# Kernel optimization log

Hardware: AMD Instinct MI355X
Metric: run time of the kernel (lower is better)

The kernel has to match this reference:

```python
import jax, jax.numpy as jnp
import numpy as np

B, N, NID, V, GH, PHI, RHO = 8, 256, 64, 128, 128, 256, 128
BN = B * N
EPS = 1e-5


def _layernorm(x, g, b):
    m = jnp.mean(x, axis=-1, keepdims=True)
    v = jnp.var(x, axis=-1, keepdims=True)
    return (x - m) * jax.lax.rsqrt(v + EPS) * g + b


def _edges(A):
    # dense adjacency -> flat batched edge list, exactly as mask.nonzero() ordering
    bidx = jnp.arange(B)[:, None, None]
    ii = jnp.arange(N)[None, :, None]
    jj = jnp.arange(N)[None, None, :]
    src = jnp.broadcast_to(bidx * N + ii, (B, N, N)).reshape(-1)  # edge_index[0] = b*N+i
    tgt = jnp.broadcast_to(bidx * N + jj, (B, N, N)).reshape(-1)  # edge_index[1] = b*N+j
    w = A.reshape(-1)
    valid = w != 0
    rel = (w > 0).astype(jnp.int32)
    return src, tgt, w, valid, rel


def _rgcn(H, src, tgt, valid, rel, Wrel, Wroot, bias):
    # torch_geometric RGCNConv: mean aggregation per relation at target + root + bias
    x_src = H[src]  # (E, d) gather
    out = H @ Wroot + bias
    for r in range(2):
        m = (valid & (rel == r)).astype(H.dtype)  # (E,)
        s = jax.ops.segment_sum(x_src * m[:, None], tgt, num_segments=BN)
        c = jax.ops.segment_sum(m, tgt, num_segments=BN)
        out = out + (s / jnp.maximum(c, 1.0)[:, None]) @ Wrel[r]
    return out


def setup_inputs() -> dict:
    key = jax.random.key(0)
    ks = jax.random.split(key, 24)
    p = lambda k, shape: jax.random.normal(k, shape, dtype=jnp.float32) * 0.02
    z = lambda *shape: jnp.zeros(shape, jnp.float32)
    return {
        "A": jax.random.normal(ks[0], (B, N, N), dtype=jnp.float32),
        "X": jax.random.normal(ks[1], (B, N, NID), dtype=jnp.float32),
        "home_mask": (jax.random.uniform(ks[2], (B, N)) > 0.5).astype(jnp.float32),
        "emb1_w": p(ks[3], (NID, V)), "emb1_b": z(V),
        "emb2_w": p(ks[4], (V, V)), "emb2_b": z(V),
        "rgcn_w_0": p(ks[5], (2, V, GH)), "rgcn_root_0": p(ks[6], (V, GH)), "rgcn_bias_0": z(GH),
        "lina_w_0": p(ks[7], (GH, GH)), "lina_b_0": z(GH),
        "linb_w_0": p(ks[8], (GH, GH)), "linb_b_0": z(GH),
        "rgcn_w_1": p(ks[9], (2, GH, GH)), "rgcn_root_1": p(ks[10], (GH, GH)), "rgcn_bias_1": z(GH),
        "lina_w_1": p(ks[11], (GH, GH)), "lina_b_1": z(GH),
        "linb_w_1": p(ks[12], (GH, GH)), "linb_b_1": z(GH),
        "norm_g": jnp.ones((GH,), jnp.float32), "norm_b": z(GH),
        "phi_w1": p(ks[13], (GH, PHI)), "phi_b1": z(PHI),
        "phi_w2": p(ks[14], (PHI, PHI)), "phi_b2": z(PHI),
        "rho_w1": p(ks[15], (PHI, RHO)), "rho_b1": z(RHO),
        "rho_w2": p(ks[16], (RHO, 1)), "rho_b2": z(1),
    }


def reference(A, X, home_mask, emb1_w, emb1_b, emb2_w, emb2_b,
              rgcn_w_0, rgcn_root_0, rgcn_bias_0, lina_w_0, lina_b_0, linb_w_0, linb_b_0,
              rgcn_w_1, rgcn_root_1, rgcn_bias_1, lina_w_1, lina_b_1, linb_w_1, linb_b_1,
              norm_g, norm_b, phi_w1, phi_b1, phi_w2, phi_b2,
              rho_w1, rho_b1, rho_w2, rho_b2):
    away_mask = 1.0 - home_mask
    H = jax.nn.relu(X @ emb1_w + emb1_b)
    H = (H @ emb2_w + emb2_b).reshape(BN, V)

    src, tgt, w, valid, rel = _edges(A)
    aw = jnp.abs(w) * valid.astype(w.dtype)  # |edge_weight|, zero for masked-out edges

    blocks = [
        (rgcn_w_0, rgcn_root_0, rgcn_bias_0, lina_w_0, lina_b_0, linb_w_0, linb_b_0),
        (rgcn_w_1, rgcn_root_1, rgcn_bias_1, lina_w_1, lina_b_1, linb_w_1, linb_b_1),
    ]
    agg = jnp.zeros_like(H)
    for (Wrel, Wroot, bias, law, lab, lbw, lbb) in blocks:
        H = H + agg
        H2 = _rgcn(H, src, tgt, valid, rel, Wrel, Wroot, bias)
        # gather-scale-scatter: agg[src] += H2[tgt] * |w|
        agg = jax.ops.segment_sum(H2[tgt] * aw[:, None], src, num_segments=BN)
        agg = jax.nn.relu(_layernorm(agg, norm_g, norm_b))  # dropout = identity (eval)
        agg = jax.nn.relu(agg @ law + lab)
        agg = agg @ lbw + lbb
    H = (H + agg).reshape(B, N, GH)

    # DeepSet phi (dropout = identity)
    h = jax.nn.relu(H @ phi_w1 + phi_b1)
    phi_out = jax.nn.relu(h @ phi_w2 + phi_b2)  # (B, N, PHI)

    home_sum = jnp.sum(phi_out * home_mask[:, :, None], axis=1)
    away_sum = jnp.sum(phi_out * away_mask[:, :, None], axis=1)

    def rho(s):
        return (jax.nn.relu(s @ rho_w1 + rho_b1) @ rho_w2 + rho_b2)[:, 0]

    out = rho(home_sum) - rho(away_sum)
    return 0.5 + 0.5 * jnp.tanh(out)  # (B,)
```

## Files before the change

### kernel.cpp

```cpp
#include <hip/hip_runtime.h>
#include <math.h>

#define NB 8

__global__ __launch_bounds__(256, 2) void k_embed(const float* __restrict__ X,
        const float* __restrict__ w1, const float* __restrict__ b1,
        const float* __restrict__ w2, const float* __restrict__ b2,
        float* __restrict__ H, float* __restrict__ pools) {
    const int r0 = blockIdx.x * 4;
    const int t = threadIdx.x, q = t & 31, u = t >> 5;
    __shared__ __align__(16) float part[4096];
    __shared__ __align__(16) float xq[256];
    __shared__ __align__(16) float h1q[512];
    if (blockIdx.x < 16) pools[blockIdx.x * 256 + t] = 0.f;
    if (t < 64) {
        float4 v;
        v.x = X[(size_t)(r0 + 0) * 64 + t];
        v.y = X[(size_t)(r0 + 1) * 64 + t];
        v.z = X[(size_t)(r0 + 2) * 64 + t];
        v.w = X[(size_t)(r0 + 3) * 64 + t];
        *(float4*)&xq[t * 4] = v;
    }
    __syncthreads();
    {
        float acc[16];
        #pragma unroll
        for (int i = 0; i < 16; ++i) acc[i] = 0.f;
        #pragma unroll
        for (int kk = 0; kk < 8; ++kk) {
            int k = u * 8 + kk;
            float4 w4 = *(const float4*)&w1[(size_t)k * 128 + q * 4];
            float wc[4] = {w4.x, w4.y, w4.z, w4.w};
            float4 x4 = *(const float4*)&xq[k * 4];
            float xr[4] = {x4.x, x4.y, x4.z, x4.w};
            #pragma unroll
            for (int r = 0; r < 4; ++r)
                #pragma unroll
                for (int c = 0; c < 4; ++c)
                    acc[r * 4 + c] = fmaf(xr[r], wc[c], acc[r * 4 + c]);
        }
        #pragma unroll
        for (int r = 0; r < 4; ++r)
            *(float4*)&part[u * 512 + r * 128 + q * 4] =
                make_float4(acc[r*4+0], acc[r*4+1], acc[r*4+2], acc[r*4+3]);
    }
    __syncthreads();
    if (t < 128) {
        int r = t >> 5, fq = t & 31;
        float4 s = *(const float4*)&b1[fq * 4];
        #pragma unroll
        for (int uu = 0; uu < 8; ++uu) {
            float4 p = *(const float4*)&part[uu * 512 + r * 128 + fq * 4];
            s.x += p.x; s.y += p.y; s.z += p.z; s.w += p.w;
        }
        h1q[(fq * 4 + 0) * 4 + r] = fmaxf(s.x, 0.f);
        h1q[(fq * 4 + 1) * 4 + r] = fmaxf(s.y, 0.f);
        h1q[(fq * 4 + 2) * 4 + r] = fmaxf(s.z, 0.f);
        h1q[(fq * 4 + 3) * 4 + r] = fmaxf(s.w, 0.f);
    }
    __syncthreads();
    {
        float a2[16];
        #pragma unroll
        for (int i = 0; i < 16; ++i) a2[i] = 0.f;
        #pragma unroll 8
        for (int kk = 0; kk < 16; ++kk) {
            int k = u * 16 + kk;
            float4 w4 = *(const float4*)&w2[(size_t)k * 128 + q * 4];
            float wc[4] = {w4.x, w4.y, w4.z, w4.w};
            float4 h4 = *(const float4*)&h1q[k * 4];
            float hr[4] = {h4.x, h4.y, h4.z, h4.w};
            #pragma unroll
            for (int r = 0; r < 4; ++r)
                #pragma unroll
                for (int c = 0; c < 4; ++c)
                    a2[r * 4 + c] = fmaf(hr[r], wc[c], a2[r * 4 + c]);
        }
        #pragma unroll
        for (int r = 0; r < 4; ++r)
            *(float4*)&part[u * 512 + r * 128 + q * 4] =
                make_float4(a2[r*4+0], a2[r*4+1], a2[r*4+2], a2[r*4+3]);
    }
    __syncthreads();
    if (t < 128) {
        int r = t >> 5, fq = t & 31;
        float4 s = *(const float4*)&b2[fq * 4];
        #pragma unroll
        for (int uu = 0; uu < 8; ++uu) {
            float4 p = *(const float4*)&part[uu * 512 + r * 128 + fq * 4];
            s.x += p.x; s.y += p.y; s.z += p.z; s.w += p.w;
        }
        *(float4*)&H[(size_t)(r0 + r) * 128 + fq * 4] = s;
    }
}

__global__ __launch_bounds__(256, 2) void k_gcn1(
        const float* __restrict__ A, const float* __restrict__ H,
        const float* __restrict__ Wrel, const float* __restrict__ Wroot,
        const float* __restrict__ bias, float* __restrict__ H2) {
    const int b  = blockIdx.x >> 6;
    const int j0 = (blockIdx.x & 63) * 4;
    const int t = threadIdx.x, q = t & 31, u = t >> 5;
    __shared__ __align__(16) float maskM[2048];
    __shared__ __align__(16) float part[8192];
    __shared__ __align__(16) float pb[1536];
    __shared__ float cntp[256];
    __shared__ float cnt[8];
    const float* Ab = A + (size_t)b * 65536;
    const float* Hb = H + (size_t)b * 32768;
    const float* W0 = Wrel;
    const float* W1 = Wrel + 16384;

    {
        float4 a = *(const float4*)(Ab + (size_t)t * 256 + j0);
        float4 m0, m1;
        m0.x = (a.x < 0.f) ? 1.f : 0.f; m1.x = (a.x > 0.f) ? 1.f : 0.f;
        m0.y = (a.y < 0.f) ? 1.f : 0.f; m1.y = (a.y > 0.f) ? 1.f : 0.f;
        m0.z = (a.z < 0.f) ? 1.f : 0.f; m1.z = (a.z > 0.f) ? 1.f : 0.f;
        m0.w = (a.w < 0.f) ? 1.f : 0.f; m1.w = (a.w > 0.f) ? 1.f : 0.f;
        *(float4*)&maskM[t * 8]     = m0;
        *(float4*)&maskM[t * 8 + 4] = m1;
    }
    __syncthreads();
    {
        int chunk = t >> 3, slot = t & 7;
        float c = 0.f;
        #pragma unroll
        for (int qq = 0; qq < 8; ++qq) c += maskM[(chunk * 8 + qq) * 8 + slot];
        cntp[slot * 32 + chunk] = c;
    }
    float acc0[16], acc1[16];
    #pragma unroll
    for (int i = 0; i < 16; ++i) { acc0[i] = 0.f; acc1[i] = 0.f; }
    #pragma unroll 8
    for (int ii = 0; ii < 32; ++ii) {
        int i = u * 32 + ii;
        float4 h4 = *(const float4*)&Hb[(size_t)i * 128 + q * 4];
        float hc[4] = {h4.x, h4.y, h4.z, h4.w};
        float4 m0 = *(const float4*)&maskM[i * 8];
        float4 m1 = *(const float4*)&maskM[i * 8 + 4];
        float mr0[4] = {m0.x, m0.y, m0.z, m0.w};
        float mr1[4] = {m1.x, m1.y, m1.z, m1.w};
        #pragma unroll
        for (int r = 0; r < 4; ++r)
            #pragma unroll
            for (int c = 0; c < 4; ++c) {
                acc0[r * 4 + c] = fmaf(mr0[r], hc[c], acc0[r * 4 + c]);
                acc1[r * 4 + c] = fmaf(mr1[r], hc[c], acc1[r * 4 + c]);
            }
    }
    #pragma unroll
    for (int r = 0; r < 4; ++r) {
        *(float4*)&part[u * 1024 + r * 128 + q * 4] =
            make_float4(acc0[r*4+0], acc0[r*4+1], acc0[r*4+2], acc0[r*4+3]);
        *(float4*)&part[u * 1024 + (4 + r) * 128 + q * 4] =
            make_float4(acc1[r*4+0], acc1[r*4+1], acc1[r*4+2], acc1[r*4+3]);
    }
    if (t < 8) {
        float s = 0.f;
        #pragma unroll
        for (int c = 0; c < 32; ++c) s += cntp[t * 32 + c];
        cnt[t] = s;
    }
    __syncthreads();
    {
        int slot = t >> 5, fq = t & 31;
        float4 s = make_float4(0.f, 0.f, 0.f, 0.f);
        #pragma unroll
        for (int uu = 0; uu < 8; ++uu) {
            float4 p = *(const float4*)&part[uu * 1024 + slot * 128 + fq * 4];
            s.x += p.x; s.y += p.y; s.z += p.z; s.w += p.w;
        }
        float rc = 1.f / fmaxf(cnt[slot], 1.f);
        pb[(fq * 4 + 0) * 12 + 4 + slot] = s.x * rc;
        pb[(fq * 4 + 1) * 12 + 4 + slot] = s.y * rc;
        pb[(fq * 4 + 2) * 12 + 4 + slot] = s.z * rc;
        pb[(fq * 4 + 3) * 12 + 4 + slot] = s.w * rc;
    }
    if (t < 128) {
        int r = t >> 5, fq = t & 31;
        float4 g4 = *(const float4*)(Hb + (size_t)(j0 + r) * 128 + fq * 4);
        pb[(fq * 4 + 0) * 12 + r] = g4.x;
        pb[(fq * 4 + 1) * 12 + r] = g4.y;
        pb[(fq * 4 + 2) * 12 + r] = g4.z;
        pb[(fq * 4 + 3) * 12 + r] = g4.w;
    }
    __syncthreads();
    float bcc[16];
    #pragma unroll
    for (int i = 0; i < 16; ++i) bcc[i] = 0.f;
    #pragma unroll 4
    for (int kk = 0; kk < 16; ++kk) {
        int k = u * 16 + kk;
        float4 wr = *(const float4*)&Wroot[(size_t)k * 128 + q * 4];
        float4 wa = *(const float4*)&W0[(size_t)k * 128 + q * 4];
        float4 wb = *(const float4*)&W1[(size_t)k * 128 + q * 4];
        float wrc[4] = {wr.x, wr.y, wr.z, wr.w};
        float wac[4] = {wa.x, wa.y, wa.z, wa.w};
        float wbc[4] = {wb.x, wb.y, wb.z, wb.w};
        float4 hv = *(const float4*)&pb[k * 12];
        float4 q0 = *(const float4*)&pb[k * 12 + 4];
        float4 q1 = *(const float4*)&pb[k * 12 + 8];
        float hr[4] = {hv.x, hv.y, hv.z, hv.w};
        float m0r[4] = {q0.x, q0.y, q0.z, q0.w};
        float m1r[4] = {q1.x, q1.y, q1.z, q1.w};
        #pragma unroll
        for (int r = 0; r < 4; ++r)
            #pragma unroll
            for (int c = 0; c < 4; ++c) {
                float v = bcc[r * 4 + c];
                v = fmaf(hr[r], wrc[c], v);
                v = fmaf(m0r[r], wac[c], v);
                v = fmaf(m1r[r], wbc[c], v);
                bcc[r * 4 + c] = v;
            }
    }
    #pragma unroll
    for (int r = 0; r < 4; ++r)
        *(float4*)&part[u * 512 + r * 128 + q * 4] =
            make_float4(bcc[r*4+0], bcc[r*4+1], bcc[r*4+2], bcc[r*4+3]);
    __syncthreads();
    if (t < 128) {
        int r = t >> 5, fq = t & 31;
        float4 s = *(const float4*)&bias[fq * 4];
        #pragma unroll
        for (int uu = 0; uu < 8; ++uu) {
            float4 p = *(const float4*)&part[uu * 512 + r * 128 + fq * 4];
            s.x += p.x; s.y += p.y; s.z += p.z; s.w += p.w;
        }
        *(float4*)&H2[(size_t)(b * 256 + j0 + r) * 128 + fq * 4] = s;
    }
}

__global__ __launch_bounds__(256, 2) void k_gcn2(
        const float* __restrict__ A, const float* __restrict__ H2,
        const float* __restrict__ g, const float* __restrict__ bta,
        const float* __restrict__ law, const float* __restrict__ lab,
        const float* __restrict__ lbw, const float* __restrict__ lbb,
        float* __restrict__ H) {
    const int b  = blockIdx.x >> 6;
    const int i0 = (blockIdx.x & 63) * 4;
    const int t = threadIdx.x, q = t & 31, u = t >> 5;
    __shared__ __align__(16) float part[4096];
    __shared__ __align__(16) float absA[1024];
    __shared__ __align__(16) float xq[512];
    __shared__ __align__(16) float uq[512];
    __shared__ float red[16];
    __shared__ float mi[8];
    const float* Ab  = A + (size_t)b * 65536;
    const float* H2b = H2 + (size_t)b * 32768;

    {
        float4 av;
        av.x = fabsf(Ab[(size_t)(i0 + 0) * 256 + t]);
        av.y = fabsf(Ab[(size_t)(i0 + 1) * 256 + t]);
        av.z = fabsf(Ab[(size_t)(i0 + 2) * 256 + t]);
        av.w = fabsf(Ab[(size_t)(i0 + 3) * 256 + t]);
        *(float4*)&absA[t * 4] = av;
    }
    __syncthreads();
    float acc[16];
    #pragma unroll
    for (int i = 0; i < 16; ++i) acc[i] = 0.f;
    #pragma unroll 8
    for (int jj = 0; jj < 32; ++jj) {
        int j = u * 32 + jj;
        float4 h4 = *(const float4*)&H2b[(size_t)j * 128 + q * 4];
        float hc[4] = {h4.x, h4.y, h4.z, h4.w};
        float4 a4 = *(const float4*)&absA[j * 4];
        float ar[4] = {a4.x, a4.y, a4.z, a4.w};
        #pragma unroll
        for (int r = 0; r < 4; ++r)
            #pragma unroll
            for (int c = 0; c < 4; ++c)
                acc[r * 4 + c] = fmaf(ar[r], hc[c], acc[r * 4 + c]);
    }
    #pragma unroll
    for (int r = 0; r < 4; ++r)
        *(float4*)&part[u * 512 + r * 128 + q * 4] =
            make_float4(acc[r*4+0], acc[r*4+1], acc[r*4+2], acc[r*4+3]);
    __syncthreads();
    float x[4] = {0.f, 0.f, 0.f, 0.f};
    if (t < 128) {
        const int wv2 = t >> 6;
        #pragma unroll
        for (int r = 0; r < 4; ++r) {
            float s = 0.f;
            #pragma unroll
            for (int uu = 0; uu < 8; ++uu) s += part[uu * 512 + r * 128 + t];
            x[r] = s;
        }
        #pragma unroll
        for (int r = 0; r < 4; ++r) {
            float s = x[r], s2 = x[r] * x[r];
            #pragma unroll
            for (int o = 32; o > 0; o >>= 1) {
                s  += __shfl_down(s, o, 64);
                s2 += __shfl_down(s2, o, 64);
            }
            if ((t & 63) == 0) {
                red[r * 4 + wv2 * 2] = s;
                red[r * 4 + wv2 * 2 + 1] = s2;
            }
        }
    }
    __syncthreads();
    if (t < 4) {
        float s  = red[t * 4] + red[t * 4 + 2];
        float s2 = red[t * 4 + 1] + red[t * 4 + 3];
        float m = s * (1.f / 128.f);
        float v = s2 * (1.f / 128.f) - m * m;
        mi[t * 2] = m;
        mi[t * 2 + 1] = rsqrtf(v + 1e-5f);
    }
    __syncthreads();
    if (t < 128) {
        float gf = g[t], bf = bta[t];
        float4 xv;
        xv.x = fmaxf((x[0] - mi[0]) * mi[1] * gf + bf, 0.f);
        xv.y = fmaxf((x[1] - mi[2]) * mi[3] * gf + bf, 0.f);
        xv.z = fmaxf((x[2] - mi[4]) * mi[5] * gf + bf, 0.f);
        xv.w = fmaxf((x[3] - mi[6]) * mi[7] * gf + bf, 0.f);
        *(float4*)&xq[t * 4] = xv;
    }
    __syncthreads();
    float u1[16];
    #pragma unroll
    for (int i = 0; i < 16; ++i) u1[i] = 0.f;
    #pragma unroll 8
    for (int kk = 0; kk < 16; ++kk) {
        int k = u * 16 + kk;
        float4 w4 = *(const float4*)&law[(size_t)k * 128 + q * 4];
        float wc[4] = {w4.x, w4.y, w4.z, w4.w};
        float4 x4 = *(const float4*)&xq[k * 4];
        float xr[4] = {x4.x, x4.y, x4.z, x4.w};
        #pragma unroll
        for (int r = 0; r < 4; ++r)
            #pragma unroll
            for (int c = 0; c < 4; ++c)
                u1[r * 4 + c] = fmaf(xr[r], wc[c], u1[r * 4 + c]);
    }
    #pragma unroll
    for (int r = 0; r < 4; ++r)
        *(float4*)&part[u * 512 + r * 128 + q * 4] =
            make_float4(u1[r*4+0], u1[r*4+1], u1[r*4+2], u1[r*4+3]);
    __syncthreads();
    if (t < 128) {
        float bb = lab[t];
        float4 uv;
        float s0 = 0.f, s1 = 0.f, s2 = 0.f, s3 = 0.f;
        #pragma unroll
        for (int uu = 0; uu < 8; ++uu) {
            s0 += part[uu * 512 + 0 * 128 + t];
            s1 += part[uu * 512 + 1 * 128 + t];
            s2 += part[uu * 512 + 2 * 128 + t];
            s3 += part[uu * 512 + 3 * 128 + t];
        }
        uv.x = fmaxf(s0 + bb, 0.f);
        uv.y = fmaxf(s1 + bb, 0.f);
        uv.z = fmaxf(s2 + bb, 0.f);
        uv.w = fmaxf(s3 + bb, 0.f);
        *(float4*)&uq[t * 4] = uv;
    }
    __syncthreads();
    float u2[16];
    #pragma unroll
    for (int i = 0; i < 16; ++i) u2[i] = 0.f;
    #pragma unroll 8
    for (int kk = 0; kk < 16; ++kk) {
        int k = u * 16 + kk;
        float4 w4 = *(const float4*)&lbw[(size_t)k * 128 + q * 4];
        float wc[4] = {w4.x, w4.y, w4.z, w4.w};
        float4 x4 = *(const float4*)&uq[k * 4];
        float xr[4] = {x4.x, x4.y, x4.z, x4.w};
        #pragma unroll
        for (int r = 0; r < 4; ++r)
            #pragma unroll
            for (int c = 0; c < 4; ++c)
                u2[r * 4 + c] = fmaf(xr[r], wc[c], u2[r * 4 + c]);
    }
    #pragma unroll
    for (int r = 0; r < 4; ++r)
        *(float4*)&part[u * 512 + r * 128 + q * 4] =
            make_float4(u2[r*4+0], u2[r*4+1], u2[r*4+2], u2[r*4+3]);
    __syncthreads();
    if (t < 128) {
        int r = t >> 5, fq = t & 31;
        float4 s = *(const float4*)&lbb[fq * 4];
        #pragma unroll
        for (int uu = 0; uu < 8; ++uu) {
            float4 p = *(const float4*)&part[uu * 512 + r * 128 + fq * 4];
            s.x += p.x; s.y += p.y; s.z += p.z; s.w += p.w;
        }
        float4 hold = *(const float4*)(H + (size_t)(b * 256 + i0 + r) * 128 + fq * 4);
        s.x += hold.x; s.y += hold.y; s.z += hold.z; s.w += hold.w;
        *(float4*)&H[(size_t)(b * 256 + i0 + r) * 128 + fq * 4] = s;
    }
}

__global__ __launch_bounds__(256, 2) void k_deepset(
        const float* __restrict__ H, const float* __restrict__ hm,
        const float* __restrict__ w1, const float* __restrict__ b1,
        const float* __restrict__ w2, const float* __restrict__ b2,
        float* __restrict__ hsum, float* __restrict__ asum) {
    const int r0 = blockIdx.x * 4;
    const int b  = blockIdx.x >> 6;
    const int t  = threadIdx.x, q = t & 63, u = t >> 6;
    __shared__ __align__(16) float part[4096];
    __shared__ __align__(16) float ph2[1024];
    __shared__ __align__(16) float hraw[512];
    __shared__ float hmv[4];
    if (t < 128) {
        float4 g4 = *(const float4*)&H[(size_t)r0 * 128 + t * 4];
        *(float4*)&hraw[t * 4] = g4;
    }
    if (t < 4) hmv[t] = hm[r0 + t];
    __syncthreads();
    float acc[16];
    #pragma unroll
    for (int i = 0; i < 16; ++i) acc[i] = 0.f;
    #pragma unroll 8
    for (int kk = 0; kk < 32; ++kk) {
        int k = u * 32 + kk;
        float4 w4 = *(const float4*)&w1[(size_t)k * 256 + q * 4];
        float wc[4] = {w4.x, w4.y, w4.z, w4.w};
        float hr[4];
        #pragma unroll
        for (int r = 0; r < 4; ++r) hr[r] = hraw[r * 128 + k];
        #pragma unroll
        for (int r = 0; r < 4; ++r)
            #pragma unroll
            for (int c = 0; c < 4; ++c)
                acc[r * 4 + c] = fmaf(hr[r], wc[c], acc[r * 4 + c]);
    }
    #pragma unroll
    for (int r = 0; r < 4; ++r)
        *(float4*)&part[u * 1024 + r * 256 + q * 4] =
            make_float4(acc[r*4+0], acc[r*4+1], acc[r*4+2], acc[r*4+3]);
    __syncthreads();
    {
        int r = t >> 6, fq = t & 63;
        float4 s = *(const float4*)&b1[fq * 4];
        #pragma unroll
        for (int uu = 0; uu < 4; ++uu) {
            float4 p = *(const float4*)&part[uu * 1024 + r * 256 + fq * 4];
            s.x += p.x; s.y += p.y; s.z += p.z; s.w += p.w;
        }
        s.x = fmaxf(s.x, 0.f); s.y = fmaxf(s.y, 0.f);
        s.z = fmaxf(s.z, 0.f); s.w = fmaxf(s.w, 0.f);
        *(float4*)&ph2[r * 256 + fq * 4] = s;
    }
    __syncthreads();
    float a2[16];
    #pragma unroll
    for (int i = 0; i < 16; ++i) a2[i] = 0.f;
    #pragma unroll 8
    for (int kk = 0; kk < 64; ++kk) {
        int k = u * 64 + kk;
        float4 w4 = *(const float4*)&w2[(size_t)k * 256 + q * 4];
        float wc[4] = {w4.x, w4.y, w4.z, w4.w};
        float pr[4];
        #pragma unroll
        for (int r = 0; r < 4; ++r) pr[r] = ph2[r * 256 + k];
        #pragma unroll
        for (int r = 0; r < 4; ++r)
            #pragma unroll
            for (int c = 0; c < 4; ++c)
                a2[r * 4 + c] = fmaf(pr[r], wc[c], a2[r * 4 + c]);
    }
    #pragma unroll
    for (int r = 0; r < 4; ++r)
        *(float4*)&part[u * 1024 + r * 256 + q * 4] =
            make_float4(a2[r*4+0], a2[r*4+1], a2[r*4+2], a2[r*4+3]);
    __syncthreads();
    {
        float bb = b2[t];
        float hp = 0.f, sp = 0.f;
        #pragma unroll
        for (int r = 0; r < 4; ++r) {
            float s = bb;
            #pragma unroll
            for (int uu = 0; uu < 4; ++uu) s += part[uu * 1024 + r * 256 + t];
            float p = fmaxf(s, 0.f);
            sp += p;
            hp = fmaf(p, hmv[r], hp);
        }
        atomicAdd(&hsum[b * 256 + t], hp);
        atomicAdd(&asum[b * 256 + t], sp - hp);
    }
}

__global__ __launch_bounds__(256) void k_rho(const float* __restrict__ hsum,
        const float* __restrict__ asum,
        const float* __restrict__ w1, const float* __restrict__ b1,
        const float* __restrict__ w2, const float* __restrict__ b2,
        float* __restrict__ out) {
    const int bIdx = blockIdx.x;
    const int t = threadIdx.x, q = t & 31, u = t >> 5;
    __shared__ __align__(16) float part[2048];
    __shared__ __align__(16) float sv[512];
    __shared__ float wsv[2];
    sv[t] = hsum[bIdx * 256 + t];
    sv[256 + t] = asum[bIdx * 256 + t];
    __syncthreads();
    float aH[4] = {0.f, 0.f, 0.f, 0.f}, aA[4] = {0.f, 0.f, 0.f, 0.f};
    #pragma unroll 8
    for (int kk = 0; kk < 32; ++kk) {
        int k = u * 32 + kk;
        float4 w4 = *(const float4*)&w1[(size_t)k * 128 + q * 4];
        float sh = sv[k], sa = sv[256 + k];
        aH[0] = fmaf(sh, w4.x, aH[0]); aA[0] = fmaf(sa, w4.x, aA[0]);
        aH[1] = fmaf(sh, w4.y, aH[1]); aA[1] = fmaf(sa, w4.y, aA[1]);
        aH[2] = fmaf(sh, w4.z, aH[2]); aA[2] = fmaf(sa, w4.z, aA[2]);
        aH[3] = fmaf(sh, w4.w, aH[3]); aA[3] = fmaf(sa, w4.w, aA[3]);
    }
    *(float4*)&part[u * 256 + q * 4]       = make_float4(aH[0], aH[1], aH[2], aH[3]);
    *(float4*)&part[u * 256 + 128 + q * 4] = make_float4(aA[0], aA[1], aA[2], aA[3]);
    __syncthreads();
    if (t < 64) {
        int vec = t >> 5, fq = t & 31;
        float4 s = make_float4(0.f, 0.f, 0.f, 0.f);
        #pragma unroll
        for (int uu = 0; uu < 8; ++uu) {
            float4 p = *(const float4*)&part[uu * 256 + vec * 128 + fq * 4];
            s.x += p.x; s.y += p.y; s.z += p.z; s.w += p.w;
        }
        float4 bb = *(const float4*)&b1[fq * 4];
        float4 w2q = *(const float4*)&w2[fq * 4];
        float p = fmaxf(s.x + bb.x, 0.f) * w2q.x
                + fmaxf(s.y + bb.y, 0.f) * w2q.y
                + fmaxf(s.z + bb.z, 0.f) * w2q.z
                + fmaxf(s.w + bb.w, 0.f) * w2q.w;
        #pragma unroll
        for (int o = 16; o > 0; o >>= 1) p += __shfl_down(p, o, 32);
        if ((t & 31) == 0) wsv[vec] = p;
    }
    __syncthreads();
    if (t == 0) out[bIdx] = 0.5f + 0.5f * tanhf(wsv[0] - wsv[1]);
}

extern "C" void kernel_launch(void* const* d_in, const int* in_sizes, int n_in,
                              void* d_out, int out_size, void* d_ws, size_t ws_size,
                              hipStream_t stream) {
    const float* A         = (const float*)d_in[0];
    const float* X         = (const float*)d_in[1];
    const float* home_mask = (const float*)d_in[2];
    const float* emb1_w    = (const float*)d_in[3];
    const float* emb1_b    = (const float*)d_in[4];
    const float* emb2_w    = (const float*)d_in[5];
    const float* emb2_b    = (const float*)d_in[6];
    const float* rgcn_w[2]    = { (const float*)d_in[7],  (const float*)d_in[14] };
    const float* rgcn_root[2] = { (const float*)d_in[8],  (const float*)d_in[15] };
    const float* rgcn_bias[2] = { (const float*)d_in[9],  (const float*)d_in[16] };
    const float* lina_w[2]    = { (const float*)d_in[10], (const float*)d_in[17] };
    const float* lina_b[2]    = { (const float*)d_in[11], (const float*)d_in[18] };
    const float* linb_w[2]    = { (const float*)d_in[12], (const float*)d_in[19] };
    const float* linb_b[2]    = { (const float*)d_in[13], (const float*)d_in[20] };
    const float* norm_g  = (const float*)d_in[21];
    const float* norm_b  = (const float*)d_in[22];
    const float* phi_w1  = (const float*)d_in[23];
    const float* phi_b1  = (const float*)d_in[24];
    const float* phi_w2  = (const float*)d_in[25];
    const float* phi_b2  = (const float*)d_in[26];
    const float* rho_w1  = (const float*)d_in[27];
    const float* rho_b1  = (const float*)d_in[28];
    const float* rho_w2  = (const float*)d_in[29];
    const float* rho_b2  = (const float*)d_in[30];
    float* out = (float*)d_out;

    float* ws   = (float*)d_ws;
    float* H    = ws;
    float* H2   = ws + 262144;
    float* hsum = ws + 524288;
    float* asum = ws + 526336;

    k_embed<<<512, 256, 0, stream>>>(X, emb1_w, emb1_b, emb2_w, emb2_b, H, hsum);

    for (int it = 0; it < 2; ++it) {
        k_gcn1<<<512, 256, 0, stream>>>(A, H, rgcn_w[it], rgcn_root[it],
                                        rgcn_bias[it], H2);
        k_gcn2<<<512, 256, 0, stream>>>(A, H2, norm_g, norm_b,
                                        lina_w[it], lina_b[it],
                                        linb_w[it], linb_b[it], H);
    }

    k_deepset<<<512, 256, 0, stream>>>(H, home_mask, phi_w1, phi_b1,
                                       phi_w2, phi_b2, hsum, asum);
    k_rho<<<NB, 256, 0, stream>>>(hsum, asum, rho_w1, rho_b1, rho_w2, rho_b2, out);
}
```

Measured before the change: 195.7 us.

## Double block size to 512 threads and halve per-thread K-split work

Every main kernel now launches with 512 threads instead of 256. Each kernel splits the reduction dimension into 16 wavefront slices instead of 8, so each thread does half the K loop, and the partial-sum buffer in shared memory doubles. The reductions are rewritten to give one scalar output per thread across all 512 threads, and gcn1 reduces its two relation accumulators in two passes to fit the buffer. The aim is more latency hiding and parallelism per block, at the cost of larger reduction overhead, more shared memory, and extra barriers.

```diff
diff --git a/kernel.cpp b/kernel.cpp
--- a/kernel.cpp
+++ b/kernel.cpp
@@ -3,16 +3,16 @@
 
 #define NB 8
 
-__global__ __launch_bounds__(256, 2) void k_embed(const float* __restrict__ X,
+__global__ __launch_bounds__(512, 4) void k_embed(const float* __restrict__ X,
         const float* __restrict__ w1, const float* __restrict__ b1,
         const float* __restrict__ w2, const float* __restrict__ b2,
         float* __restrict__ H, float* __restrict__ pools) {
     const int r0 = blockIdx.x * 4;
     const int t = threadIdx.x, q = t & 31, u = t >> 5;
-    __shared__ __align__(16) float part[4096];
+    __shared__ __align__(16) float part[8192];
     __shared__ __align__(16) float xq[256];
     __shared__ __align__(16) float h1q[512];
-    if (blockIdx.x < 16) pools[blockIdx.x * 256 + t] = 0.f;
+    if (blockIdx.x < 8) pools[blockIdx.x * 512 + t] = 0.f;
     if (t < 64) {
         float4 v;
         v.x = X[(size_t)(r0 + 0) * 64 + t];
@@ -27,8 +27,8 @@
         #pragma unroll
         for (int i = 0; i < 16; ++i) acc[i] = 0.f;
         #pragma unroll
-        for (int kk = 0; kk < 8; ++kk) {
-            int k = u * 8 + kk;
+        for (int kk = 0; kk < 4; ++kk) {
+            int k = u * 4 + kk;
             float4 w4 = *(const float4*)&w1[(size_t)k * 128 + q * 4];
             float wc[4] = {w4.x, w4.y, w4.z, w4.w};
             float4 x4 = *(const float4*)&xq[k * 4];
@@ -45,27 +45,21 @@
                 make_float4(acc[r*4+0], acc[r*4+1], acc[r*4+2], acc[r*4+3]);
     }
     __syncthreads();
-    if (t < 128) {
-        int r = t >> 5, fq = t & 31;
-        float4 s = *(const float4*)&b1[fq * 4];
-        #pragma unroll
-        for (int uu = 0; uu < 8; ++uu) {
-            float4 p = *(const float4*)&part[uu * 512 + r * 128 + fq * 4];
-            s.x += p.x; s.y += p.y; s.z += p.z; s.w += p.w;
-        }
-        h1q[(fq * 4 + 0) * 4 + r] = fmaxf(s.x, 0.f);
-        h1q[(fq * 4 + 1) * 4 + r] = fmaxf(s.y, 0.f);
-        h1q[(fq * 4 + 2) * 4 + r] = fmaxf(s.z, 0.f);
-        h1q[(fq * 4 + 3) * 4 + r] = fmaxf(s.w, 0.f);
+    {
+        int r = t >> 7, f = t & 127;
+        float s = b1[f];
+        #pragma unroll
+        for (int uu = 0; uu < 16; ++uu) s += part[uu * 512 + r * 128 + f];
+        h1q[f * 4 + r] = fmaxf(s, 0.f);
     }
     __syncthreads();
     {
         float a2[16];
         #pragma unroll
         for (int i = 0; i < 16; ++i) a2[i] = 0.f;
-        #pragma unroll 8
-        for (int kk = 0; kk < 16; ++kk) {
-            int k = u * 16 + kk;
+        #pragma unroll
+        for (int kk = 0; kk < 8; ++kk) {
+            int k = u * 8 + kk;
             float4 w4 = *(const float4*)&w2[(size_t)k * 128 + q * 4];
             float wc[4] = {w4.x, w4.y, w4.z, w4.w};
             float4 h4 = *(const float4*)&h1q[k * 4];
@@ -82,19 +76,16 @@
                 make_float4(a2[r*4+0], a2[r*4+1], a2[r*4+2], a2[r*4+3]);
     }
     __syncthreads();
-    if (t < 128) {
-        int r = t >> 5, fq = t & 31;
-        float4 s = *(const float4*)&b2[fq * 4];
-        #pragma unroll
-        for (int uu = 0; uu < 8; ++uu) {
-            float4 p = *(const float4*)&part[uu * 512 + r * 128 + fq * 4];
-            s.x += p.x; s.y += p.y; s.z += p.z; s.w += p.w;
-        }
-        *(float4*)&H[(size_t)(r0 + r) * 128 + fq * 4] = s;
+    {
+        int r = t >> 7, f = t & 127;
+        float s = b2[f];
+        #pragma unroll
+        for (int uu = 0; uu < 16; ++uu) s += part[uu * 512 + r * 128 + f];
+        H[(size_t)(r0 + r) * 128 + f] = s;
     }
 }
 
-__global__ __launch_bounds__(256, 2) void k_gcn1(
+__global__ __launch_bounds__(512, 4) void k_gcn1(
         const float* __restrict__ A, const float* __restrict__ H,
         const float* __restrict__ Wrel, const float* __restrict__ Wroot,
         const float* __restrict__ bias, float* __restrict__ H2) {
@@ -111,7 +102,7 @@
     const float* W0 = Wrel;
     const float* W1 = Wrel + 16384;
 
-    {
+    if (t < 256) {
         float4 a = *(const float4*)(Ab + (size_t)t * 256 + j0);
         float4 m0, m1;
         m0.x = (a.x < 0.f) ? 1.f : 0.f; m1.x = (a.x > 0.f) ? 1.f : 0.f;
@@ -122,7 +113,7 @@
         *(float4*)&maskM[t * 8 + 4] = m1;
     }
     __syncthreads();
-    {
+    if (t < 256) {
         int chunk = t >> 3, slot = t & 7;
         float c = 0.f;
         #pragma unroll
@@ -133,8 +124,8 @@
     #pragma unroll
     for (int i = 0; i < 16; ++i) { acc0[i] = 0.f; acc1[i] = 0.f; }
     #pragma unroll 8
-    for (int ii = 0; ii < 32; ++ii) {
-        int i = u * 32 + ii;
+    for (int ii = 0; ii < 16; ++ii) {
+        int i = u * 16 + ii;
         float4 h4 = *(const float4*)&Hb[(size_t)i * 128 + q * 4];
         float hc[4] = {h4.x, h4.y, h4.z, h4.w};
         float4 m0 = *(const float4*)&maskM[i * 8];
@@ -150,12 +141,9 @@
             }
     }
     #pragma unroll
-    for (int r = 0; r < 4; ++r) {
-        *(float4*)&part[u * 1024 + r * 128 + q * 4] =
+    for (int r = 0; r < 4; ++r)
+        *(float4*)&part[u * 512 + r * 128 + q * 4] =
             make_float4(acc0[r*4+0], acc0[r*4+1], acc0[r*4+2], acc0[r*4+3]);
-        *(float4*)&part[u * 1024 + (4 + r) * 128 + q * 4] =
-            make_float4(acc1[r*4+0], acc1[r*4+1], acc1[r*4+2], acc1[r*4+3]);
-    }
     if (t < 8) {
         float s = 0.f;
         #pragma unroll
@@ -164,18 +152,24 @@
     }
     __syncthreads();
     {
-        int slot = t >> 5, fq = t & 31;
-        float4 s = make_float4(0.f, 0.f, 0.f, 0.f);
-        #pragma unroll
-        for (int uu = 0; uu < 8; ++uu) {
-            float4 p = *(const float4*)&part[uu * 1024 + slot * 128 + fq * 4];
-            s.x += p.x; s.y += p.y; s.z += p.z; s.w += p.w;
-        }
-        float rc = 1.f / fmaxf(cnt[slot], 1.f);
-        pb[(fq * 4 + 0) * 12 + 4 + slot] = s.x * rc;
-        pb[(fq * 4 + 1) * 12 + 4 + slot] = s.y * rc;
-        pb[(fq * 4 + 2) * 12 + 4 + slot] = s.z * rc;
-        pb[(fq * 4 + 3) * 12 + 4 + slot] = s.w * rc;
+        int r = t >> 7, f = t & 127;
+        float s = 0.f;
+        #pragma unroll
+        for (int uu = 0; uu < 16; ++uu) s += part[uu * 512 + r * 128 + f];
+        pb[f * 12 + 4 + r] = s * (1.f / fmaxf(cnt[r], 1.f));
+    }
+    __syncthreads();
+    #pragma unroll
+    for (int r = 0; r < 4; ++r)
+        *(float4*)&part[u * 512 + r * 128 + q * 4] =
+            make_float4(acc1[r*4+0], acc1[r*4+1], acc1[r*4+2], acc1[r*4+3]);
+    __syncthreads();
+    {
+        int r = t >> 7, f = t & 127;
+        float s = 0.f;
+        #pragma unroll
+        for (int uu = 0; uu < 16; ++uu) s += part[uu * 512 + r * 128 + f];
+        pb[f * 12 + 8 + r] = s * (1.f / fmaxf(cnt[4 + r], 1.f));
     }
     if (t < 128) {
         int r = t >> 5, fq = t & 31;
@@ -190,8 +184,8 @@
     #pragma unroll
     for (int i = 0; i < 16; ++i) bcc[i] = 0.f;
     #pragma unroll 4
-    for (int kk = 0; kk < 16; ++kk) {
-        int k = u * 16 + kk;
+    for (int kk = 0; kk < 8; ++kk) {
+        int k = u * 8 + kk;
         float4 wr = *(const float4*)&Wroot[(size_t)k * 128 + q * 4];
         float4 wa = *(const float4*)&W0[(size_t)k * 128 + q * 4];
         float4 wb = *(const float4*)&W1[(size_t)k * 128 + q * 4];
@@ -220,19 +214,16 @@
         *(float4*)&part[u * 512 + r * 128 + q * 4] =
             make_float4(bcc[r*4+0], bcc[r*4+1], bcc[r*4+2], bcc[r*4+3]);
     __syncthreads();
-    if (t < 128) {
-        int r = t >> 5, fq = t & 31;
-        float4 s = *(const float4*)&bias[fq * 4];
-        #pragma unroll
-        for (int uu = 0; uu < 8; ++uu) {
-            float4 p = *(const float4*)&part[uu * 512 + r * 128 + fq * 4];
-            s.x += p.x; s.y += p.y; s.z += p.z; s.w += p.w;
-        }
-        *(float4*)&H2[(size_t)(b * 256 + j0 + r) * 128 + fq * 4] = s;
+    {
+        int r = t >> 7, f = t & 127;
+        float s = bias[f];
+        #pragma unroll
+        for (int uu = 0; uu < 16; ++uu) s += part[uu * 512 + r * 128 + f];
+        H2[(size_t)(b * 256 + j0 + r) * 128 + f] = s;
     }
 }
 
-__global__ __launch_bounds__(256, 2) void k_gcn2(
+__global__ __launch_bounds__(512, 4) void k_gcn2(
         const float* __restrict__ A, const float* __restrict__ H2,
         const float* __restrict__ g, const float* __restrict__ bta,
         const float* __restrict__ law, const float* __restrict__ lab,
@@ -241,7 +232,7 @@
     const int b  = blockIdx.x >> 6;
     const int i0 = (blockIdx.x & 63) * 4;
     const int t = threadIdx.x, q = t & 31, u = t >> 5;
-    __shared__ __align__(16) float part[4096];
+    __shared__ __align__(16) float part[8192];
     __shared__ __align__(16) float absA[1024];
     __shared__ __align__(16) float xq[512];
     __shared__ __align__(16) float uq[512];
@@ -250,7 +241,7 @@
     const float* Ab  = A + (size_t)b * 65536;
     const float* H2b = H2 + (size_t)b * 32768;
 
-    {
+    if (t < 256) {
         float4 av;
         av.x = fabsf(Ab[(size_t)(i0 + 0) * 256 + t]);
         av.y = fabsf(Ab[(size_t)(i0 + 1) * 256 + t]);
@@ -263,8 +254,8 @@
     #pragma unroll
     for (int i = 0; i < 16; ++i) acc[i] = 0.f;
     #pragma unroll 8
-    for (int jj = 0; jj < 32; ++jj) {
-        int j = u * 32 + jj;
+    for (int jj = 0; jj < 16; ++jj) {
+        int j = u * 16 + jj;
         float4 h4 = *(const float4*)&H2b[(size_t)j * 128 + q * 4];
         float hc[4] = {h4.x, h4.y, h4.z, h4.w};
         float4 a4 = *(const float4*)&absA[j * 4];
@@ -280,33 +271,29 @@
         *(float4*)&part[u * 512 + r * 128 + q * 4] =
             make_float4(acc[r*4+0], acc[r*4+1], acc[r*4+2], acc[r*4+3]);
     __syncthreads();
-    float x[4] = {0.f, 0.f, 0.f, 0.f};
-    if (t < 128) {
-        const int wv2 = t >> 6;
-        #pragma unroll
-        for (int r = 0; r < 4; ++r) {
-            float s = 0.f;
-            #pragma unroll
-            for (int uu = 0; uu < 8; ++uu) s += part[uu * 512 + r * 128 + t];
-            x[r] = s;
-        }
-        #pragma unroll
-        for (int r = 0; r < 4; ++r) {
-            float s = x[r], s2 = x[r] * x[r];
-            #pragma unroll
-            for (int o = 32; o > 0; o >>= 1) {
-                s  += __shfl_down(s, o, 64);
-                s2 += __shfl_down(s2, o, 64);
-            }
-            if ((t & 63) == 0) {
-                red[r * 4 + wv2 * 2] = s;
-                red[r * 4 + wv2 * 2 + 1] = s2;
-            }
+    const int rr = t >> 7, ff = t & 127;
+    float x;
+    {
+        float s = 0.f;
+        #pragma unroll
+        for (int uu = 0; uu < 16; ++uu) s += part[uu * 512 + rr * 128 + ff];
+        x = s;
+        float s2 = x * x;
+        float sw = x;
+        #pragma unroll
+        for (int o = 32; o > 0; o >>= 1) {
+            sw += __shfl_down(sw, o, 64);
+            s2 += __shfl_down(s2, o, 64);
+        }
+        int w = (t >> 6) & 1;
+        if ((t & 63) == 0) {
+            red[(rr * 2 + w) * 2]     = sw;
+            red[(rr * 2 + w) * 2 + 1] = s2;
         }
     }
     __syncthreads();
     if (t < 4) {
-        float s  = red[t * 4] + red[t * 4 + 2];
+        float s  = red[t * 4]     + red[t * 4 + 2];
         float s2 = red[t * 4 + 1] + red[t * 4 + 3];
         float m = s * (1.f / 128.f);
         float v = s2 * (1.f / 128.f) - m * m;
@@ -314,22 +301,14 @@
         mi[t * 2 + 1] = rsqrtf(v + 1e-5f);
     }
     __syncthreads();
-    if (t < 128) {
-        float gf = g[t], bf = bta[t];
-        float4 xv;
-        xv.x = fmaxf((x[0] - mi[0]) * mi[1] * gf + bf, 0.f);
-        xv.y = fmaxf((x[1] - mi[2]) * mi[3] * gf + bf, 0.f);
-        xv.z = fmaxf((x[2] - mi[4]) * mi[5] * gf + bf, 0.f);
-        xv.w = fmaxf((x[3] - mi[6]) * mi[7] * gf + bf, 0.f);
-        *(float4*)&xq[t * 4] = xv;
-    }
+    xq[ff * 4 + rr] = fmaxf((x - mi[rr * 2]) * mi[rr * 2 + 1] * g[ff] + bta[ff], 0.f);
     __syncthreads();
     float u1[16];
     #pragma unroll
     for (int i = 0; i < 16; ++i) u1[i] = 0.f;
-    #pragma unroll 8
-    for (int kk = 0; kk < 16; ++kk) {
-        int k = u * 16 + kk;
+    #pragma unroll
+    for (int kk = 0; kk < 8; ++kk) {
+        int k = u * 8 + kk;
         float4 w4 = *(const float4*)&law[(size_t)k * 128 + q * 4];
         float wc[4] = {w4.x, w4.y, w4.z, w4.w};
         float4 x4 = *(const float4*)&xq[k * 4];
@@ -345,30 +324,19 @@
         *(float4*)&part[u * 512 + r * 128 + q * 4] =
             make_float4(u1[r*4+0], u1[r*4+1], u1[r*4+2], u1[r*4+3]);
     __syncthreads();
-    if (t < 128) {
-        float bb = lab[t];
-        float4 uv;
-        float s0 = 0.f, s1 = 0.f, s2 = 0.f, s3 = 0.f;
-        #pragma unroll
-        for (int uu = 0; uu < 8; ++uu) {
-            s0 += part[uu * 512 + 0 * 128 + t];
-            s1 += part[uu * 512 + 1 * 128 + t];
-            s2 += part[uu * 512 + 2 * 128 + t];
-            s3 += part[uu * 512 + 3 * 128 + t];
-        }
-        uv.x = fmaxf(s0 + bb, 0.f);
-        uv.y = fmaxf(s1 + bb, 0.f);
-        uv.z = fmaxf(s2 + bb, 0.f);
-        uv.w = fmaxf(s3 + bb, 0.f);
-        *(float4*)&uq[t * 4] = uv;
+    {
+        float s = lab[ff];
+        #pragma unroll
+        for (int uu = 0; uu < 16; ++uu) s += part[uu * 512 + rr * 128 + ff];
+        uq[ff * 4 + rr] = fmaxf(s, 0.f);
     }
     __syncthreads();
     float u2[16];
     #pragma unroll
     for (int i = 0; i < 16; ++i) u2[i] = 0.f;
-    #pragma unroll 8
-    for (int kk = 0; kk < 16; ++kk) {
-        int k = u * 16 + kk;
+    #pragma unroll
+    for (int kk = 0; kk < 8; ++kk) {
+        int k = u * 8 + kk;
         float4 w4 = *(const float4*)&lbw[(size_t)k * 128 + q * 4];
         float wc[4] = {w4.x, w4.y, w4.z, w4.w};
         float4 x4 = *(const float4*)&uq[k * 4];
@@ -384,21 +352,16 @@
         *(float4*)&part[u * 512 + r * 128 + q * 4] =
             make_float4(u2[r*4+0], u2[r*4+1], u2[r*4+2], u2[r*4+3]);
     __syncthreads();
-    if (t < 128) {
-        int r = t >> 5, fq = t & 31;
-        float4 s = *(const float4*)&lbb[fq * 4];
-        #pragma unroll
-        for (int uu = 0; uu < 8; ++uu) {
-            float4 p = *(const float4*)&part[uu * 512 + r * 128 + fq * 4];
-            s.x += p.x; s.y += p.y; s.z += p.z; s.w += p.w;
-        }
-        float4 hold = *(const float4*)(H + (size_t)(b * 256 + i0 + r) * 128 + fq * 4);
-        s.x += hold.x; s.y += hold.y; s.z += hold.z; s.w += hold.w;
-        *(float4*)&H[(size_t)(b * 256 + i0 + r) * 128 + fq * 4] = s;
+    {
+        float s = lbb[ff];
+        #pragma unroll
+        for (int uu = 0; uu < 16; ++uu) s += part[uu * 512 + rr * 128 + ff];
+        size_t idx = (size_t)(b * 256 + i0 + rr) * 128 + ff;
+        H[idx] = s + H[idx];
     }
 }
 
-__global__ __launch_bounds__(256, 2) void k_deepset(
+__global__ __launch_bounds__(512, 4) void k_deepset(
         const float* __restrict__ H, const float* __restrict__ hm,
         const float* __restrict__ w1, const float* __restrict__ b1,
         const float* __restrict__ w2, const float* __restrict__ b2,
@@ -406,7 +369,7 @@
     const int r0 = blockIdx.x * 4;
     const int b  = blockIdx.x >> 6;
     const int t  = threadIdx.x, q = t & 63, u = t >> 6;
-    __shared__ __align__(16) float part[4096];
+    __shared__ __align__(16) float part[8192];
     __shared__ __align__(16) float ph2[1024];
     __shared__ __align__(16) float hraw[512];
     __shared__ float hmv[4];
@@ -420,8 +383,8 @@
     #pragma unroll
     for (int i = 0; i < 16; ++i) acc[i] = 0.f;
     #pragma unroll 8
-    for (int kk = 0; kk < 32; ++kk) {
-        int k = u * 32 + kk;
+    for (int kk = 0; kk < 16; ++kk) {
+        int k = u * 16 + kk;
         float4 w4 = *(const float4*)&w1[(size_t)k * 256 + q * 4];
         float wc[4] = {w4.x, w4.y, w4.z, w4.w};
         float hr[4];
@@ -439,24 +402,23 @@
             make_float4(acc[r*4+0], acc[r*4+1], acc[r*4+2], acc[r*4+3]);
     __syncthreads();
     {
-        int r = t >> 6, fq = t & 63;
-        float4 s = *(const float4*)&b1[fq * 4];
-        #pragma unroll
-        for (int uu = 0; uu < 4; ++uu) {
-            float4 p = *(const float4*)&part[uu * 1024 + r * 256 + fq * 4];
-            s.x += p.x; s.y += p.y; s.z += p.z; s.w += p.w;
-        }
-        s.x = fmaxf(s.x, 0.f); s.y = fmaxf(s.y, 0.f);
-        s.z = fmaxf(s.z, 0.f); s.w = fmaxf(s.w, 0.f);
-        *(float4*)&ph2[r * 256 + fq * 4] = s;
+        #pragma unroll
+        for (int e = 0; e < 2; ++e) {
+            int idx = e * 512 + t;
+            int r = idx >> 8, f = idx & 255;
+            float s = b1[f];
+            #pragma unroll
+            for (int uu = 0; uu < 8; ++uu) s += part[uu * 1024 + r * 256 + f];
+            ph2[r * 256 + f] = fmaxf(s, 0.f);
+        }
     }
     __syncthreads();
     float a2[16];
     #pragma unroll
     for (int i = 0; i < 16; ++i) a2[i] = 0.f;
     #pragma unroll 8
-    for (int kk = 0; kk < 64; ++kk) {
-        int k = u * 64 + kk;
+    for (int kk = 0; kk < 32; ++kk) {
+        int k = u * 32 + kk;
         float4 w4 = *(const float4*)&w2[(size_t)k * 256 + q * 4];
         float wc[4] = {w4.x, w4.y, w4.z, w4.w};
         float pr[4];
@@ -473,14 +435,14 @@
         *(float4*)&part[u * 1024 + r * 256 + q * 4] =
             make_float4(a2[r*4+0], a2[r*4+1], a2[r*4+2], a2[r*4+3]);
     __syncthreads();
-    {
+    if (t < 256) {
         float bb = b2[t];
         float hp = 0.f, sp = 0.f;
         #pragma unroll
         for (int r = 0; r < 4; ++r) {
             float s = bb;
             #pragma unroll
-            for (int uu = 0; uu < 4; ++uu) s += part[uu * 1024 + r * 256 + t];
+            for (int uu = 0; uu < 8; ++uu) s += part[uu * 1024 + r * 256 + t];
             float p = fmaxf(s, 0.f);
             sp += p;
             hp = fmaf(p, hmv[r], hp);
@@ -574,17 +536,17 @@
     float* hsum = ws + 524288;
     float* asum = ws + 526336;
 
-    k_embed<<<512, 256, 0, stream>>>(X, emb1_w, emb1_b, emb2_w, emb2_b, H, hsum);
+    k_embed<<<512, 512, 0, stream>>>(X, emb1_w, emb1_b, emb2_w, emb2_b, H, hsum);
 
     for (int it = 0; it < 2; ++it) {
-        k_gcn1<<<512, 256, 0, stream>>>(A, H, rgcn_w[it], rgcn_root[it],
+        k_gcn1<<<512, 512, 0, stream>>>(A, H, rgcn_w[it], rgcn_root[it],
                                         rgcn_bias[it], H2);
-        k_gcn2<<<512, 256, 0, stream>>>(A, H2, norm_g, norm_b,
+        k_gcn2<<<512, 512, 0, stream>>>(A, H2, norm_g, norm_b,
                                         lina_w[it], lina_b[it],
                                         linb_w[it], linb_b[it], H);
     }
 
-    k_deepset<<<512, 256, 0, stream>>>(H, home_mask, phi_w1, phi_b1,
+    k_deepset<<<512, 512, 0, stream>>>(H, home_mask, phi_w1, phi_b1,
                                        phi_w2, phi_b2, hsum, asum);
     k_rho<<<NB, 256, 0, stream>>>(hsum, asum, rho_w1, rho_b1, rho_w2, rho_b2, out);
 }
```

After: 189.3 us. -3.3%, faster.
